# Performance work log

Measured on AMD Instinct MI355X. Metric: run time of the kernel, lower is better.

The kernel has to match this reference:

```python
import jax, jax.numpy as jnp
import numpy as np

B = 256        # graphs per batch
M = 512        # atoms per complex (uniform; batch = arange(N)//M)
K_NN = 33      # max_num_neighbors + 1 (loop=True includes self edge)
RADIUS = 5.0   # interaction_radius


def setup_inputs() -> dict:
    key = jax.random.key(0)
    # coords scaled so a 5 A radius keeps a realistic fraction of edges
    pos = jax.random.normal(key, (B * M, 3), dtype=jnp.float32) * 8.0
    batch = (jnp.arange(B * M, dtype=jnp.int32) // M).astype(jnp.int32)
    return {"pos": pos, "batch": batch}


def _safe_sqrt(x):
    # sqrt with well-defined value (and grad) at 0; forward-identical to sqrt
    pos_x = jnp.where(x > 0, x, 1.0)
    return jnp.where(x > 0, jnp.sqrt(pos_x), 0.0)


def reference(pos, batch):
    # batch is sorted with uniform graph size M, so grouping == reshape.
    p = pos.reshape(B, M, 3)
    sq = jnp.sum(p * p, axis=-1)                                  # [B, M]
    # squared pairwise distances per graph via ||x||^2+||y||^2-2xy
    d2 = sq[:, :, None] + sq[:, None, :] - 2.0 * jnp.einsum("bmd,bnd->bmn", p, p)
    d2 = jnp.maximum(d2, 0.0)                                     # [B, M, M]
    # k nearest (incl. self, d2=0) == knn_graph(pos, k, batch, loop=True)
    _, nbr = jax.lax.top_k(-d2, K_NN)                             # [B, M, K]
    base = (jnp.arange(B, dtype=jnp.int32) * M)[:, None, None]
    src = (nbr.astype(jnp.int32) + base).reshape(-1)              # neighbor (source) ids
    dst = jnp.repeat(jnp.arange(B * M, dtype=jnp.int32), K_NN)    # center (target) ids
    edge_index = jnp.stack([src, dst])                            # [2, B*M*K]
    # recompute distances on gathered endpoints, as the torch code does
    diff = pos[src] - pos[dst]                                    # [E, 3]
    dist = _safe_sqrt(jnp.sum(diff * diff, axis=-1))              # [E]
    mask = dist <= RADIUS                                         # radius filter (kept as mask: jit-static shapes)
    return edge_index, dist, mask
```

## Files before the change

### kernel.cpp

```cpp
#include <hip/hip_runtime.h>
#include <stdint.h>

#define BATCH    256
#define MPTS     512
#define KNN      33
#define RADIUS_F 5.0f
#define EDGES    (BATCH * MPTS * KNN)

#define BLOCKS_PER_GRAPH 8
#define ROWS_PER_BLOCK   64
#define THREADS          256
#define WAVES_PER_BLOCK  4
#define SLOT_STRIDE      72

typedef float f32x2 __attribute__((ext_vector_type(2)));

#if defined(__has_builtin)
#if __has_builtin(__builtin_amdgcn_permlane16_swap)
#define HAVE_PL16 1
#endif
#if __has_builtin(__builtin_amdgcn_permlane32_swap)
#define HAVE_PL32 1
#endif
#if __has_builtin(__builtin_elementwise_fma)
#define HAVE_PKFMA 1
#endif
#endif

template <int J>
static __device__ __forceinline__ uint32_t shx32(uint32_t x) {
    if constexpr (J == 1) {
        return (uint32_t)__builtin_amdgcn_update_dpp(0, (int)x, 0xB1, 0xF, 0xF, false);
    } else if constexpr (J == 2) {
        return (uint32_t)__builtin_amdgcn_update_dpp(0, (int)x, 0x4E, 0xF, 0xF, false);
    } else if constexpr (J == 4) {
        const uint32_t a = (uint32_t)__builtin_amdgcn_update_dpp(0, (int)x, 0x104, 0xF, 0xF, false);
        const uint32_t b = (uint32_t)__builtin_amdgcn_update_dpp(0, (int)x, 0x114, 0xF, 0xF, false);
        return ((threadIdx.x & 4u) == 0u) ? a : b;
    } else if constexpr (J == 8) {
        return (uint32_t)__builtin_amdgcn_update_dpp(0, (int)x, 0x128, 0xF, 0xF, false);
    } else if constexpr (J == 16) {
#ifdef HAVE_PL16
        auto r = __builtin_amdgcn_permlane16_swap((int)x, (int)x, false, false);
        return ((uint32_t)r[0] ^ (uint32_t)r[1]) ^ x;
#else
        return (uint32_t)__builtin_amdgcn_ds_swizzle((int)x, 0x401F);
#endif
    } else {
#ifdef HAVE_PL32
        auto r = __builtin_amdgcn_permlane32_swap((int)x, (int)x, false, false);
        return ((uint32_t)r[0] ^ (uint32_t)r[1]) ^ x;
#else
        return (uint32_t)__shfl_xor((int)x, 32, 64);
#endif
    }
}

template <int J>
static __device__ __forceinline__ void ce32(uint32_t& v, bool lowJ, bool up) {
    const uint32_t p = shx32<J>(v);
    const bool km = (lowJ == up);
    v = ((v < p) == km) ? v : p;
}

static __device__ __forceinline__ void bsort64d(uint32_t& a, uint32_t& b,
        bool l1, bool l2, bool l4, bool l8, bool l16, bool l32) {
#define C2(J, L, U) do { ce32<J>(a, L, U); ce32<J>(b, L, U); } while (0)
    C2(1, l1, l2);
    C2(2, l2, l4);   C2(1, l1, l4);
    C2(4, l4, l8);   C2(2, l2, l8);   C2(1, l1, l8);
    C2(8, l8, l16);  C2(4, l4, l16);  C2(2, l2, l16);  C2(1, l1, l16);
    C2(16, l16, l32); C2(8, l8, l32); C2(4, l4, l32);  C2(2, l2, l32); C2(1, l1, l32);
    C2(32, l32, true); C2(16, l16, true); C2(8, l8, true);
    C2(4, l4, true);   C2(2, l2, true);   C2(1, l1, true);
#undef C2
}

template <int CTRL, int ROWM>
static __device__ __forceinline__ uint32_t dpp_min(uint32_t x) {
    const uint32_t t = (uint32_t)__builtin_amdgcn_update_dpp(
        (int)0xFFFFFFFFu, (int)x, CTRL, ROWM, 0xF, false);
    return t < x ? t : x;
}
template <int CTRL, int ROWM>
static __device__ __forceinline__ uint32_t dpp_max(uint32_t x) {
    const uint32_t t = (uint32_t)__builtin_amdgcn_update_dpp(
        0, (int)x, CTRL, ROWM, 0xF, false);
    return t > x ? t : x;
}
static __device__ __forceinline__ uint32_t reduce63_min(uint32_t x) {
    x = dpp_min<0x111, 0xF>(x);
    x = dpp_min<0x112, 0xF>(x);
    x = dpp_min<0x114, 0xF>(x);
    x = dpp_min<0x118, 0xF>(x);
    x = dpp_min<0x142, 0xA>(x);
    x = dpp_min<0x143, 0xC>(x);
    return x;
}
static __device__ __forceinline__ uint32_t reduce63_max(uint32_t x) {
    x = dpp_max<0x111, 0xF>(x);
    x = dpp_max<0x112, 0xF>(x);
    x = dpp_max<0x114, 0xF>(x);
    x = dpp_max<0x118, 0xF>(x);
    x = dpp_max<0x142, 0xA>(x);
    x = dpp_max<0x143, 0xC>(x);
    return x;
}

static __device__ __forceinline__ uint32_t wave_incl_scan(uint32_t x) {
    x += (uint32_t)__builtin_amdgcn_update_dpp(0, (int)x, 0x111, 0xF, 0xF, false);
    x += (uint32_t)__builtin_amdgcn_update_dpp(0, (int)x, 0x112, 0xF, 0xF, false);
    x += (uint32_t)__builtin_amdgcn_update_dpp(0, (int)x, 0x114, 0xF, 0xF, false);
    x += (uint32_t)__builtin_amdgcn_update_dpp(0, (int)x, 0x118, 0xF, 0xF, false);
    x += (uint32_t)__builtin_amdgcn_update_dpp(0, (int)x, 0x142, 0xA, 0xF, false);
    x += (uint32_t)__builtin_amdgcn_update_dpp(0, (int)x, 0x143, 0xC, 0xF, false);
    return x;
}

__global__ void __launch_bounds__(THREADS)
InteractionModule_50483045597845_kernel(const float* __restrict__ pos,
                                        float* __restrict__ out) {
    __shared__ float4 spt[MPTS];
    __shared__ uint32_t slots[WAVES_PER_BLOCK * 2][SLOT_STRIDE];

    const int graph = blockIdx.x / BLOCKS_PER_GRAPH;
    const int slice = blockIdx.x - graph * BLOCKS_PER_GRAPH;
    const int tid   = (int)threadIdx.x;

    for (int p = tid; p < MPTS; p += THREADS) {
        const float* pp = pos + (size_t)(graph * MPTS + p) * 3;
        const float x = pp[0], y = pp[1], z = pp[2];
        const float sq = __builtin_fmaf(x, x, __builtin_fmaf(y, y, __fmul_rn(z, z)));
        spt[p] = make_float4(x, y, z, sq);
    }
    __syncthreads();

    const int lane = tid & 63;
    const int wave = tid >> 6;

    const bool l1  = (lane & 1) == 0;
    const bool l2  = (lane & 2) == 0;
    const bool l4  = (lane & 4) == 0;
    const bool l8  = (lane & 8) == 0;
    const bool l16 = (lane & 16) == 0;
    const bool l32 = (lane & 32) == 0;

    auto emitRow = [&](uint32_t v0, const float4 pc, int mRow) {
        if (lane < KNN) {
            const int kept  = (int)(v0 & 0x1FFu);
            const float4 q  = spt[kept];
            const float dx  = __fsub_rn(q.x, pc.x);
            const float dy  = __fsub_rn(q.y, pc.y);
            const float dz  = __fsub_rn(q.z, pc.z);
            const float ss  = __fadd_rn(__fadd_rn(__fmul_rn(dx, dx),
                                                  __fmul_rn(dy, dy)),
                                        __fmul_rn(dz, dz));
            const float dist  = (ss > 0.0f) ? __fsqrt_rn(ss) : 0.0f;
            const float maskv = (dist <= RADIUS_F) ? 1.0f : 0.0f;
            const size_t e    = (size_t)mRow * KNN + (size_t)lane;
            out[e]                     = (float)(graph * MPTS + kept);
            out[(size_t)EDGES + e]     = (float)mRow;
            out[2 * (size_t)EDGES + e] = dist;
            out[3 * (size_t)EDGES + e] = maskv;
        }
    };

    auto refineRow = [&](const uint32_t* sk, uint32_t& P,
                         uint32_t& cnt, uint32_t& incl) {
        uint32_t lo = 0u, hi = P;
        while (lo < hi) {
            const uint32_t mid = (lo + hi) >> 1;
            uint32_t c = 0;
            #pragma unroll
            for (int j = 0; j < 8; ++j) c += (sk[j] <= mid) ? 1u : 0u;
            const uint32_t t =
                (uint32_t)__builtin_amdgcn_readlane((int)wave_incl_scan(c), 63);
            if (t < KNN) lo = mid + 1; else hi = mid;
        }
        P = hi;
        cnt = 0;
        #pragma unroll
        for (int j = 0; j < 8; ++j) cnt += (sk[j] <= P) ? 1u : 0u;
        incl = wave_incl_scan(cnt);
    };

    #pragma unroll 1
    for (int it = 0; it < ROWS_PER_BLOCK / (WAVES_PER_BLOCK * 2); ++it) {
        const int mA = slice * ROWS_PER_BLOCK + it * (WAVES_PER_BLOCK * 2) + wave;
        const int mB = mA + WAVES_PER_BLOCK;

        const float4 pa = spt[mA];
        const float4 pb = spt[mB];

        uint32_t sA[8], sB[8];
        {
#ifdef HAVE_PKFMA
            const f32x2 px = {pa.x, pb.x}, py = {pa.y, pb.y};
            const f32x2 pz = {pa.z, pb.z}, pw = {pa.w, pb.w};
            const f32x2 m2 = {-2.0f, -2.0f};
#endif
            #pragma unroll
            for (int j = 0; j < 8; ++j) {
                const int n = lane + (j << 6);
                const float4 q = spt[n];
#ifdef HAVE_PKFMA
                const f32x2 qx = {q.x, q.x}, qy = {q.y, q.y};
                const f32x2 qz = {q.z, q.z}, qw = {q.w, q.w};
                const f32x2 dot = __builtin_elementwise_fma(px, qx,
                                  __builtin_elementwise_fma(py, qy, pz * qz));
                const f32x2 d2  = __builtin_elementwise_fma(m2, dot, pw + qw);
                const float d2A = fmaxf(d2[0], 0.0f);
                const float d2B = fmaxf(d2[1], 0.0f);
#else
                const float dotA = __builtin_fmaf(pa.x, q.x,
                                   __builtin_fmaf(pa.y, q.y, __fmul_rn(pa.z, q.z)));
                const float dotB = __builtin_fmaf(pb.x, q.x,
                                   __builtin_fmaf(pb.y, q.y, __fmul_rn(pb.z, q.z)));
                const float d2A = fmaxf(__builtin_fmaf(-2.0f, dotA, __fadd_rn(pa.w, q.w)), 0.0f);
                const float d2B = fmaxf(__builtin_fmaf(-2.0f, dotB, __fadd_rn(pb.w, q.w)), 0.0f);
#endif
                sA[j] = (__float_as_uint(d2A) & 0xFFFFFE00u) | (uint32_t)n;
                sB[j] = (__float_as_uint(d2B) & 0xFFFFFE00u) | (uint32_t)n;
            }
        }

        uint32_t hA = sA[0], hB = sB[0];
        #pragma unroll
        for (int j = 1; j < 8; ++j) {
            hA = sA[j] < hA ? sA[j] : hA;
            hB = sB[j] < hB ? sB[j] : hB;
        }

        uint32_t loA = (uint32_t)__builtin_amdgcn_readlane((int)reduce63_min(hA), 63);
        uint32_t hiA_ = (uint32_t)__builtin_amdgcn_readlane((int)reduce63_max(hA), 63);
        uint32_t loB = (uint32_t)__builtin_amdgcn_readlane((int)reduce63_min(hB), 63);
        uint32_t hiB_ = (uint32_t)__builtin_amdgcn_readlane((int)reduce63_max(hB), 63);
        while (loA < hiA_ || loB < hiB_) {
            const uint32_t midA = loA + ((hiA_ - loA) >> 1);
            const uint32_t midB = loB + ((hiB_ - loB) >> 1);
            const int cA = __popcll(__ballot(hA <= midA));
            const int cB = __popcll(__ballot(hB <= midB));
            const bool openA = loA < hiA_, okA = cA >= KNN;
            const bool openB = loB < hiB_, okB = cB >= KNN;
            const uint32_t nloA = okA ? ((cA <= KNN + 3) ? midA : loA) : (midA + 1u);
            const uint32_t nloB = okB ? ((cB <= KNN + 3) ? midB : loB) : (midB + 1u);
            const uint32_t nhiA = okA ? midA : hiA_;
            const uint32_t nhiB = okB ? midB : hiB_;
            loA = openA ? nloA : loA;  hiA_ = openA ? nhiA : hiA_;
            loB = openB ? nloB : loB;  hiB_ = openB ? nhiB : hiB_;
        }
        uint32_t PA = hiA_;
        uint32_t PB = hiB_;

        uint32_t cntA = 0, cntB = 0;
        #pragma unroll
        for (int j = 0; j < 8; ++j) {
            cntA += (sA[j] <= PA) ? 1u : 0u;
            cntB += (sB[j] <= PB) ? 1u : 0u;
        }
        uint32_t inclA = wave_incl_scan(cntA);
        uint32_t inclB = wave_incl_scan(cntB);
        const uint32_t totalA = (uint32_t)__builtin_amdgcn_readlane((int)inclA, 63);
        const uint32_t totalB = (uint32_t)__builtin_amdgcn_readlane((int)inclB, 63);

        if (__builtin_expect(totalA > 64u, 0)) refineRow(sA, PA, cntA, inclA);
        if (__builtin_expect(totalB > 64u, 0)) refineRow(sB, PB, cntB, inclB);

        const int rA = wave;
        const int rB = wave + WAVES_PER_BLOCK;
        const int mRowA = graph * MPTS + mA;
        const int mRowB = graph * MPTS + mB;

        slots[rA][lane] = 0xFFFFFFFFu;
        slots[rB][lane] = 0xFFFFFFFFu;
        uint32_t dA = inclA - cntA;
        uint32_t dB = inclB - cntB;
        #pragma unroll
        for (int j = 0; j < 8; ++j) {
            const bool svA = (sA[j] <= PA);
            const bool svB = (sB[j] <= PB);
            if (svA) slots[rA][dA] = sA[j];
            if (svB) slots[rB][dB] = sB[j];
            dA += svA ? 1u : 0u;
            dB += svB ? 1u : 0u;
        }

        uint32_t vA = slots[rA][lane];
        uint32_t vB = slots[rB][lane];
        bsort64d(vA, vB, l1, l2, l4, l8, l16, l32);
        emitRow(vA, pa, mRowA);
        emitRow(vB, pb, mRowB);
    }
}

extern "C" void kernel_launch(void* const* d_in, const int* in_sizes, int n_in,
                              void* d_out, int out_size, void* d_ws, size_t ws_size,
                              hipStream_t stream) {
    (void)in_sizes; (void)n_in; (void)out_size; (void)d_ws; (void)ws_size;
    const float* pos = (const float*)d_in[0];
    float*       out = (float*)d_out;
    hipLaunchKernelGGL(InteractionModule_50483045597845_kernel,
                       dim3(BATCH * BLOCKS_PER_GRAPH), dim3(THREADS), 0, stream,
                       pos, out);
}
```

Baseline: 161.0 us.

## Split graphs across more blocks, fix bisection steps, and pack dual-row emission

Doubles blocks per graph with half the rows each and sets a launch-bounds occupancy hint, to raise parallelism and overlap. Replaces the data-dependent bisection loop with a fixed 13-step unrolled search, drops the clamp to zero, and turns the predicated LDS scatter into unconditional writes into a padded dump region. The two-row emit now uses 64 lanes for 66 outputs through a bpermute instead of two passes with 33 active lanes each. It also adds a per-wave sleep stagger at start. Dropping the clamp and using a fixed step count may change tie or negative-distance handling, and the sleeps add latency.

```diff
diff --git a/kernel.cpp b/kernel.cpp
--- a/kernel.cpp
+++ b/kernel.cpp
@@ -7,11 +7,12 @@
 #define RADIUS_F 5.0f
 #define EDGES    (BATCH * MPTS * KNN)
 
-#define BLOCKS_PER_GRAPH 8
-#define ROWS_PER_BLOCK   64
+#define BLOCKS_PER_GRAPH 16
+#define ROWS_PER_BLOCK   32
 #define THREADS          256
 #define WAVES_PER_BLOCK  4
-#define SLOT_STRIDE      72
+#define SLOT_STRIDE      130
+#define BSTEPS           13
 
 typedef float f32x2 __attribute__((ext_vector_type(2)));
 
@@ -117,7 +118,7 @@
     return x;
 }
 
-__global__ void __launch_bounds__(THREADS)
+__global__ void __launch_bounds__(THREADS, 8)
 InteractionModule_50483045597845_kernel(const float* __restrict__ pos,
                                         float* __restrict__ out) {
     __shared__ float4 spt[MPTS];
@@ -126,9 +127,10 @@
     const int graph = blockIdx.x / BLOCKS_PER_GRAPH;
     const int slice = blockIdx.x - graph * BLOCKS_PER_GRAPH;
     const int tid   = (int)threadIdx.x;
+    const int gbase = graph * MPTS;
 
     for (int p = tid; p < MPTS; p += THREADS) {
-        const float* pp = pos + (size_t)(graph * MPTS + p) * 3;
+        const float* pp = pos + (size_t)(gbase + p) * 3;
         const float x = pp[0], y = pp[1], z = pp[2];
         const float sq = __builtin_fmaf(x, x, __builtin_fmaf(y, y, __fmul_rn(z, z)));
         spt[p] = make_float4(x, y, z, sq);
@@ -137,6 +139,12 @@
 
     const int lane = tid & 63;
     const int wave = tid >> 6;
+
+    {
+        uint32_t stag = ((((uint32_t)blockIdx.x) * 2654435761u) >> 29) + (uint32_t)wave;
+        stag &= 7u;
+        for (uint32_t i = 0; i < stag; ++i) __builtin_amdgcn_s_sleep(2);
+    }
 
     const bool l1  = (lane & 1) == 0;
     const bool l2  = (lane & 2) == 0;
@@ -145,31 +153,29 @@
     const bool l16 = (lane & 16) == 0;
     const bool l32 = (lane & 32) == 0;
 
-    auto emitRow = [&](uint32_t v0, const float4 pc, int mRow) {
-        if (lane < KNN) {
-            const int kept  = (int)(v0 & 0x1FFu);
-            const float4 q  = spt[kept];
-            const float dx  = __fsub_rn(q.x, pc.x);
-            const float dy  = __fsub_rn(q.y, pc.y);
-            const float dz  = __fsub_rn(q.z, pc.z);
-            const float ss  = __fadd_rn(__fadd_rn(__fmul_rn(dx, dx),
-                                                  __fmul_rn(dy, dy)),
-                                        __fmul_rn(dz, dz));
-            const float dist  = (ss > 0.0f) ? __fsqrt_rn(ss) : 0.0f;
-            const float maskv = (dist <= RADIUS_F) ? 1.0f : 0.0f;
-            const size_t e    = (size_t)mRow * KNN + (size_t)lane;
-            out[e]                     = (float)(graph * MPTS + kept);
-            out[(size_t)EDGES + e]     = (float)mRow;
-            out[2 * (size_t)EDGES + e] = dist;
-            out[3 * (size_t)EDGES + e] = maskv;
-        }
+    auto emitOne = [&](uint32_t key, float cx, float cy, float cz, int mRow, int k) {
+        const int kept  = (int)(key & 0x1FFu);
+        const float4 q  = spt[kept];
+        const float dx  = __fsub_rn(q.x, cx);
+        const float dy  = __fsub_rn(q.y, cy);
+        const float dz  = __fsub_rn(q.z, cz);
+        const float ss  = __fadd_rn(__fadd_rn(__fmul_rn(dx, dx),
+                                              __fmul_rn(dy, dy)),
+                                    __fmul_rn(dz, dz));
+        const float dist  = (ss > 0.0f) ? __fsqrt_rn(ss) : 0.0f;
+        const float maskv = (dist <= RADIUS_F) ? 1.0f : 0.0f;
+        const size_t e    = (size_t)mRow * KNN + (size_t)k;
+        out[e]                     = (float)(gbase + kept);
+        out[(size_t)EDGES + e]     = (float)mRow;
+        out[2 * (size_t)EDGES + e] = dist;
+        out[3 * (size_t)EDGES + e] = maskv;
     };
 
     auto refineRow = [&](const uint32_t* sk, uint32_t& P,
                          uint32_t& cnt, uint32_t& incl) {
         uint32_t lo = 0u, hi = P;
         while (lo < hi) {
-            const uint32_t mid = (lo + hi) >> 1;
+            const uint32_t mid = lo + ((hi - lo) >> 1);
             uint32_t c = 0;
             #pragma unroll
             for (int j = 0; j < 8; ++j) c += (sk[j] <= mid) ? 1u : 0u;
@@ -209,15 +215,15 @@
                 const f32x2 dot = __builtin_elementwise_fma(px, qx,
                                   __builtin_elementwise_fma(py, qy, pz * qz));
                 const f32x2 d2  = __builtin_elementwise_fma(m2, dot, pw + qw);
-                const float d2A = fmaxf(d2[0], 0.0f);
-                const float d2B = fmaxf(d2[1], 0.0f);
+                const float d2A = d2[0];
+                const float d2B = d2[1];
 #else
                 const float dotA = __builtin_fmaf(pa.x, q.x,
                                    __builtin_fmaf(pa.y, q.y, __fmul_rn(pa.z, q.z)));
                 const float dotB = __builtin_fmaf(pb.x, q.x,
                                    __builtin_fmaf(pb.y, q.y, __fmul_rn(pb.z, q.z)));
-                const float d2A = fmaxf(__builtin_fmaf(-2.0f, dotA, __fadd_rn(pa.w, q.w)), 0.0f);
-                const float d2B = fmaxf(__builtin_fmaf(-2.0f, dotB, __fadd_rn(pb.w, q.w)), 0.0f);
+                const float d2A = __builtin_fmaf(-2.0f, dotA, __fadd_rn(pa.w, q.w));
+                const float d2B = __builtin_fmaf(-2.0f, dotB, __fadd_rn(pb.w, q.w));
 #endif
                 sA[j] = (__float_as_uint(d2A) & 0xFFFFFE00u) | (uint32_t)n;
                 sB[j] = (__float_as_uint(d2B) & 0xFFFFFE00u) | (uint32_t)n;
@@ -231,23 +237,22 @@
             hB = sB[j] < hB ? sB[j] : hB;
         }
 
-        uint32_t loA = (uint32_t)__builtin_amdgcn_readlane((int)reduce63_min(hA), 63);
+        uint32_t loA  = (uint32_t)__builtin_amdgcn_readlane((int)reduce63_min(hA), 63);
         uint32_t hiA_ = (uint32_t)__builtin_amdgcn_readlane((int)reduce63_max(hA), 63);
-        uint32_t loB = (uint32_t)__builtin_amdgcn_readlane((int)reduce63_min(hB), 63);
+        uint32_t loB  = (uint32_t)__builtin_amdgcn_readlane((int)reduce63_min(hB), 63);
         uint32_t hiB_ = (uint32_t)__builtin_amdgcn_readlane((int)reduce63_max(hB), 63);
-        while (loA < hiA_ || loB < hiB_) {
+        #pragma unroll
+        for (int step = 0; step < BSTEPS; ++step) {
             const uint32_t midA = loA + ((hiA_ - loA) >> 1);
             const uint32_t midB = loB + ((hiB_ - loB) >> 1);
             const int cA = __popcll(__ballot(hA <= midA));
             const int cB = __popcll(__ballot(hB <= midB));
-            const bool openA = loA < hiA_, okA = cA >= KNN;
-            const bool openB = loB < hiB_, okB = cB >= KNN;
-            const uint32_t nloA = okA ? ((cA <= KNN + 3) ? midA : loA) : (midA + 1u);
-            const uint32_t nloB = okB ? ((cB <= KNN + 3) ? midB : loB) : (midB + 1u);
-            const uint32_t nhiA = okA ? midA : hiA_;
-            const uint32_t nhiB = okB ? midB : hiB_;
-            loA = openA ? nloA : loA;  hiA_ = openA ? nhiA : hiA_;
-            loB = openB ? nloB : loB;  hiB_ = openB ? nhiB : hiB_;
+            const bool okA = cA >= KNN;
+            const bool okB = cB >= KNN;
+            loA  = okA ? loA  : (midA + 1u);
+            hiA_ = okA ? midA : hiA_;
+            loB  = okB ? loB  : (midB + 1u);
+            hiB_ = okB ? midB : hiB_;
         }
         uint32_t PA = hiA_;
         uint32_t PB = hiB_;
@@ -268,8 +273,8 @@
 
         const int rA = wave;
         const int rB = wave + WAVES_PER_BLOCK;
-        const int mRowA = graph * MPTS + mA;
-        const int mRowB = graph * MPTS + mB;
+        const int mRowA = gbase + mA;
+        const int mRowB = gbase + mB;
 
         slots[rA][lane] = 0xFFFFFFFFu;
         slots[rB][lane] = 0xFFFFFFFFu;
@@ -279,8 +284,10 @@
         for (int j = 0; j < 8; ++j) {
             const bool svA = (sA[j] <= PA);
             const bool svB = (sB[j] <= PB);
-            if (svA) slots[rA][dA] = sA[j];
-            if (svB) slots[rB][dB] = sB[j];
+            const uint32_t wA_ = svA ? dA : (64u + (uint32_t)lane);
+            const uint32_t wB_ = svB ? dB : (64u + (uint32_t)lane);
+            slots[rA][wA_] = sA[j];
+            slots[rB][wB_] = sB[j];
             dA += svA ? 1u : 0u;
             dB += svB ? 1u : 0u;
         }
@@ -288,8 +295,22 @@
         uint32_t vA = slots[rA][lane];
         uint32_t vB = slots[rB][lane];
         bsort64d(vA, vB, l1, l2, l4, l8, l16, l32);
-        emitRow(vA, pa, mRowA);
-        emitRow(vB, pb, mRowB);
+
+        {
+            const bool isA = (lane < KNN);
+            const int  k1  = isA ? lane : (lane - KNN);
+            const uint32_t vBs = (uint32_t)__builtin_amdgcn_ds_bpermute(
+                (((lane - KNN) & 63) << 2), (int)vB);
+            const uint32_t key1 = isA ? vA : vBs;
+            const float cx = isA ? pa.x : pb.x;
+            const float cy = isA ? pa.y : pb.y;
+            const float cz = isA ? pa.z : pb.z;
+            const int mRow1 = isA ? mRowA : mRowB;
+            emitOne(key1, cx, cy, cz, mRow1, k1);
+            if ((unsigned)(lane - 31) < 2u) {
+                emitOne(vB, pb.x, pb.y, pb.z, mRowB, lane);
+            }
+        }
     }
 }
 
```

After: 217.9 us. 1.35x slower.
